# Kernel optimization log

Hardware: AMD Instinct MI355X
Metric: run time of the kernel (lower is better)

The kernel has to match this reference:

```python
import jax, jax.numpy as jnp
import numpy as np

N_ATOMS = 20000
N_PAIRS = 320000
F = 128


def setup_inputs() -> dict:
    key = jax.random.key(0)
    k1, k2, k3, k4, k5 = jax.random.split(key, 5)
    atomic_embedding = jax.random.normal(k1, (N_ATOMS, F), dtype=jnp.float32)
    pairlist = jax.random.randint(k2, (2, N_PAIRS), 0, N_ATOMS)
    f_ij_cutoff = jax.random.uniform(k3, (N_PAIRS, 1), dtype=jnp.float32)
    r_ij = jax.random.normal(k4, (N_PAIRS, 3), dtype=jnp.float32)
    # nn.Linear(F, F) parameters
    W = jax.random.normal(k5, (F, F), dtype=jnp.float32) * (1.0 / np.sqrt(F))
    b = jnp.zeros((F,), dtype=jnp.float32)
    return {"atomic_embedding": atomic_embedding, "pairlist": pairlist,
            "f_ij_cutoff": f_ij_cutoff, "r_ij": r_ij, "W": W, "b": b}


def reference(atomic_embedding, pairlist, f_ij_cutoff, r_ij, W, b):
    n_atoms = atomic_embedding.shape[0]
    idx_i, idx_j = pairlist[0], pairlist[1]
    # gather neighbor embeddings and apply cutoff weight: [P, F]
    a_j = atomic_embedding[idx_j]
    weighted = f_ij_cutoff * a_j
    # scatter-add radial contributions: [N, F]
    radial = jax.ops.segment_sum(weighted, idx_i, num_segments=n_atoms)
    # unit vectors: [P, 3]
    u_ij = r_ij / jnp.linalg.norm(r_ij, axis=1, keepdims=True)
    # outer product per pair: [P, 3, F]
    uwe = u_ij[:, :, None] * weighted[:, None, :]
    # linear layer applied on last dim (y = x @ W^T + b): [P, 3, F]
    transformed = jnp.einsum('pcf,gf->pcg', uwe, W) + b
    # scatter-add vector contributions: [N, 3, F]
    vec = jax.ops.segment_sum(transformed, idx_i, num_segments=n_atoms)
    # norm over the 3 spatial components (eps guards atoms with no pairs): [N, F]
    vector_norms = jnp.sqrt(jnp.sum(vec * vec, axis=1) + 1e-12)
    # combined message: [N, 2F]
    return jnp.concatenate([vector_norms, radial], axis=-1)
```

## Files before the change

kernel.cpp:

```cpp
#include <hip/hip_runtime.h>
#include <hip/hip_bf16.h>

#define FDIM 128
#define CAP 48

typedef short bf16x8 __attribute__((ext_vector_type(8)));
typedef float f32x4  __attribute__((ext_vector_type(4)));

__device__ inline short f2bf_rne(float x) {
    unsigned u = __builtin_bit_cast(unsigned, x);
    u += 0x7FFFu + ((u >> 16) & 1u);
    return (short)(u >> 16);
}
__device__ inline float readlane_f(float v, int l) {
    return __builtin_bit_cast(float, __builtin_amdgcn_readlane(__builtin_bit_cast(int, v), l));
}

__global__ void fill_repack_kernel(const int* __restrict__ pair, const float* __restrict__ fcut,
                                   const float* __restrict__ rij, int* __restrict__ cursor,
                                   int4* __restrict__ rec, const float* __restrict__ W,
                                   short* __restrict__ Wf, int P, int PB) {
    int bx = blockIdx.x;
    if (bx >= PB) {
        int idx = (bx - PB) * 256 + threadIdx.x;
        if (idx < 16384) {
            int j  = idx & 7;
            int l  = (idx >> 3) & 63;
            int tk = idx >> 9;
            int g  = (tk >> 2) * 16 + (l & 15);
            int f  = (tk & 3) * 32 + (l >> 4) * 8 + j;
            Wf[idx] = f2bf_rne(W[g * FDIM + f]);
        }
        return;
    }
    int p = bx * 256 + threadIdx.x;
    if (p >= P) return;
    int i = pair[p], j = pair[P + p];
    float fc = fcut[p];
    float rx = rij[3 * p], ry = rij[3 * p + 1], rz = rij[3 * p + 2];
    float inv = rsqrtf(rx * rx + ry * ry + rz * rz);
    int slot = atomicAdd(&cursor[i], 1);
    if (slot < CAP) {
        int base = (i * CAP + slot) * 2;
        rec[base]     = make_int4(j, 0, 0, 0);
        ((float4*)rec)[base + 1] = make_float4(rx * inv, ry * inv, rz * inv, fc);
    }
}

__global__ __launch_bounds__(256) void fused_kernel(
    const float* __restrict__ A, const int4* __restrict__ rec,
    const int* __restrict__ cursor, const bf16x8* __restrict__ Wfv,
    const float* __restrict__ b, float* __restrict__ out, int N)
{
    __shared__ float sl[4][12][132];
    int wave = __builtin_amdgcn_readfirstlane(threadIdx.x >> 6);
    int lane = threadIdx.x & 63;
    int i0 = blockIdx.x * 16 + wave * 4;
    const float2* A2 = (const float2*)A;
    float cntf[4];

#pragma unroll
    for (int a = 0; a < 4; ++a) {
        int i = i0 + a;
        if (i >= N) { cntf[a] = 0.f; continue; }
        int cnt = __builtin_amdgcn_readfirstlane(min(cursor[i], CAP));
        cntf[a] = (float)cnt;
        int jreg = 0; float ux = 0.f, uy = 0.f, uz = 0.f, fc = 0.f;
        if (lane < cnt) {
            int base = (i * CAP + lane) * 2;
            int4  rj = rec[base];
            float4 ru = ((const float4*)rec)[base + 1];
            jreg = rj.x; ux = ru.x; uy = ru.y; uz = ru.z; fc = ru.w;
        }
        float2 ar = {0.f, 0.f}, ax = {0.f, 0.f}, ay = {0.f, 0.f}, az = {0.f, 0.f};
        for (int k0 = 0; k0 < cnt; k0 += 8) {
            int sj[8]; float sx[8], sy[8], sz[8], sf[8]; float2 aa[8];
#pragma unroll
            for (int q = 0; q < 8; ++q) {
                sj[q] = __builtin_amdgcn_readlane(jreg, k0 + q);
                sx[q] = readlane_f(ux, k0 + q);
                sy[q] = readlane_f(uy, k0 + q);
                sz[q] = readlane_f(uz, k0 + q);
                sf[q] = readlane_f(fc, k0 + q);
            }
#pragma unroll
            for (int q = 0; q < 8; ++q) aa[q] = A2[(size_t)sj[q] * 64 + lane];
#pragma unroll
            for (int q = 0; q < 8; ++q) {
                float wx = sf[q] * aa[q].x, wy = sf[q] * aa[q].y;
                ar.x += wx; ar.y += wy;
                ax.x = fmaf(sx[q], wx, ax.x); ax.y = fmaf(sx[q], wy, ax.y);
                ay.x = fmaf(sy[q], wx, ay.x); ay.y = fmaf(sy[q], wy, ay.y);
                az.x = fmaf(sz[q], wx, az.x); az.y = fmaf(sz[q], wy, az.y);
            }
        }
        ((float2*)&sl[wave][a * 3 + 0][0])[lane] = ax;
        ((float2*)&sl[wave][a * 3 + 1][0])[lane] = ay;
        ((float2*)&sl[wave][a * 3 + 2][0])[lane] = az;
        ((float2*)(out + (size_t)i * 256 + 128))[lane] = ar;
    }

    int m = lane & 15, quad = lane >> 4;
    int mc = min(m, 11);
    bf16x8 a_hi[4], a_lo[4];
    const float* arow = &sl[wave][mc][quad * 8];
#pragma unroll
    for (int kc = 0; kc < 4; ++kc) {
        float4 x0 = *(const float4*)(arow + kc * 32);
        float4 x1 = *(const float4*)(arow + kc * 32 + 4);
        float v[8] = {x0.x, x0.y, x0.z, x0.w, x1.x, x1.y, x1.z, x1.w};
#pragma unroll
        for (int e = 0; e < 8; ++e) {
            float xv = (m < 12) ? v[e] : 0.f;
            unsigned u = __builtin_bit_cast(unsigned, xv);
            float hf = __builtin_bit_cast(float, u & 0xFFFF0000u);
            float r = xv - hf;
            a_hi[kc][e] = (short)(u >> 16);
            a_lo[kc][e] = (short)(__builtin_bit_cast(unsigned, r) >> 16);
        }
    }
    int row0 = quad * 4;
#pragma unroll
    for (int t = 0; t < 8; ++t) {
        f32x4 acc = {0.f, 0.f, 0.f, 0.f};
#pragma unroll
        for (int kc = 0; kc < 4; ++kc) {
            bf16x8 bw = Wfv[(t * 4 + kc) * 64 + lane];
            acc = __builtin_amdgcn_mfma_f32_16x16x32_bf16(a_hi[kc], bw, acc, 0, 0, 0);
            acc = __builtin_amdgcn_mfma_f32_16x16x32_bf16(a_lo[kc], bw, acc, 0, 0, 0);
        }
#pragma unroll
        for (int reg = 0; reg < 4; ++reg) {
            int r = row0 + reg;
            if (r < 12) sl[wave][r][t * 16 + m] = acc[reg];
        }
    }

    float bg0 = b[lane], bg1 = b[lane + 64];
#pragma unroll
    for (int a = 0; a < 4; ++a) {
        int i = i0 + a;
        if (i >= N) continue;
        float t0 = cntf[a] * bg0, t1 = cntf[a] * bg1;
        float v00 = sl[wave][a * 3 + 0][lane] + t0;
        float v10 = sl[wave][a * 3 + 1][lane] + t0;
        float v20 = sl[wave][a * 3 + 2][lane] + t0;
        float v01 = sl[wave][a * 3 + 0][lane + 64] + t1;
        float v11 = sl[wave][a * 3 + 1][lane + 64] + t1;
        float v21 = sl[wave][a * 3 + 2][lane + 64] + t1;
        out[(size_t)i * 256 + lane]      = sqrtf(fmaf(v00, v00, fmaf(v10, v10, fmaf(v20, v20, 1e-12f))));
        out[(size_t)i * 256 + lane + 64] = sqrtf(fmaf(v01, v01, fmaf(v11, v11, fmaf(v21, v21, 1e-12f))));
    }
}

extern "C" void kernel_launch(void* const* d_in, const int* in_sizes, int n_in,
                              void* d_out, int out_size, void* d_ws, size_t ws_size,
                              hipStream_t stream) {
    const float* A    = (const float*)d_in[0];
    const int*   pair = (const int*)d_in[1];
    const float* fcut = (const float*)d_in[2];
    const float* rij  = (const float*)d_in[3];
    const float* W    = (const float*)d_in[4];
    const float* b    = (const float*)d_in[5];
    float* out = (float*)d_out;

    int N = in_sizes[0] / FDIM;
    int P = in_sizes[1] / 2;

    int Npad = ((N + 63) / 64) * 64;
    int*   cursor = (int*)d_ws;
    int4*  rec    = (int4*)(cursor + Npad);
    short* Wf     = (short*)((char*)rec + (size_t)N * CAP * 32);

    int PB = (P + 255) / 256;
    hipMemsetAsync(cursor, 0, (size_t)N * sizeof(int), stream);
    fill_repack_kernel<<<PB + 64, 256, 0, stream>>>(pair, fcut, rij, cursor, rec, W, Wf, P, PB);
    fused_kernel<<<(N + 15) / 16, 256, 0, stream>>>(A, rec, cursor, (const bf16x8*)Wf, b, out, N);
}
```

Before: 127.5 us.

## Shrink bucket records to (j, pair index) and gather geometry in fused kernel

The fill kernel now writes only an 8-byte record (neighbor index, pair index) per slot instead of a 32-byte record holding the unit vector and cutoff. The fused kernel gathers fcut and r_ij by pair index and computes the normalisation itself. All four atoms' records are loaded up front to expose more memory parallelism, and the gather loop is unrolled to 16 neighbors. This cuts scatter-write and reread traffic for the records, at the cost of random gathers of fcut and r_ij in the main kernel and higher register pressure.

```diff
diff --git a/kernel.cpp b/kernel.cpp
--- a/kernel.cpp
+++ b/kernel.cpp
@@ -16,9 +16,8 @@
     return __builtin_bit_cast(float, __builtin_amdgcn_readlane(__builtin_bit_cast(int, v), l));
 }
 
-__global__ void fill_repack_kernel(const int* __restrict__ pair, const float* __restrict__ fcut,
-                                   const float* __restrict__ rij, int* __restrict__ cursor,
-                                   int4* __restrict__ rec, const float* __restrict__ W,
+__global__ void fill_repack_kernel(const int* __restrict__ pair, int* __restrict__ cursor,
+                                   int2* __restrict__ rec, const float* __restrict__ W,
                                    short* __restrict__ Wf, int P, int PB) {
     int bx = blockIdx.x;
     if (bx >= PB) {
@@ -35,21 +34,15 @@
     }
     int p = bx * 256 + threadIdx.x;
     if (p >= P) return;
-    int i = pair[p], j = pair[P + p];
-    float fc = fcut[p];
-    float rx = rij[3 * p], ry = rij[3 * p + 1], rz = rij[3 * p + 2];
-    float inv = rsqrtf(rx * rx + ry * ry + rz * rz);
+    int i = pair[p];
     int slot = atomicAdd(&cursor[i], 1);
-    if (slot < CAP) {
-        int base = (i * CAP + slot) * 2;
-        rec[base]     = make_int4(j, 0, 0, 0);
-        ((float4*)rec)[base + 1] = make_float4(rx * inv, ry * inv, rz * inv, fc);
-    }
+    if (slot < CAP) rec[i * CAP + slot] = make_int2(pair[P + p], p);
 }
 
 __global__ __launch_bounds__(256) void fused_kernel(
-    const float* __restrict__ A, const int4* __restrict__ rec,
-    const int* __restrict__ cursor, const bf16x8* __restrict__ Wfv,
+    const float* __restrict__ A, const int2* __restrict__ rec,
+    const int* __restrict__ cursor, const float* __restrict__ fcut,
+    const float* __restrict__ rij, const bf16x8* __restrict__ Wfv,
     const float* __restrict__ b, float* __restrict__ out, int N)
 {
     __shared__ float sl[4][12][132];
@@ -57,41 +50,56 @@
     int lane = threadIdx.x & 63;
     int i0 = blockIdx.x * 16 + wave * 4;
     const float2* A2 = (const float2*)A;
-    float cntf[4];
 
+    int cnts[4], jreg[4], preg[4];
+    float uxr[4], uyr[4], uzr[4], fcr[4];
 #pragma unroll
     for (int a = 0; a < 4; ++a) {
         int i = i0 + a;
-        if (i >= N) { cntf[a] = 0.f; continue; }
-        int cnt = __builtin_amdgcn_readfirstlane(min(cursor[i], CAP));
-        cntf[a] = (float)cnt;
-        int jreg = 0; float ux = 0.f, uy = 0.f, uz = 0.f, fc = 0.f;
-        if (lane < cnt) {
-            int base = (i * CAP + lane) * 2;
-            int4  rj = rec[base];
-            float4 ru = ((const float4*)rec)[base + 1];
-            jreg = rj.x; ux = ru.x; uy = ru.y; uz = ru.z; fc = ru.w;
+        int cnt = (i < N) ? min(cursor[i], CAP) : 0;
+        cnt = __builtin_amdgcn_readfirstlane(cnt);
+        cnts[a] = cnt;
+        int2 r = make_int2(0, 0);
+        if (lane < cnt) r = rec[i * CAP + lane];
+        jreg[a] = r.x; preg[a] = r.y;
+    }
+#pragma unroll
+    for (int a = 0; a < 4; ++a) {
+        float fc = 0.f, rx = 0.f, ry = 0.f, rz = 1.f;
+        if (lane < cnts[a]) {
+            int p = preg[a];
+            fc = fcut[p];
+            rx = rij[3 * p]; ry = rij[3 * p + 1]; rz = rij[3 * p + 2];
         }
+        float inv = rsqrtf(rx * rx + ry * ry + rz * rz);
+        uxr[a] = rx * inv; uyr[a] = ry * inv; uzr[a] = rz * inv; fcr[a] = fc;
+    }
+
+    float cntf[4];
+#pragma unroll
+    for (int a = 0; a < 4; ++a) {
+        int i = i0 + a;
+        cntf[a] = (float)cnts[a];
+        if (i >= N) continue;
+        int cnt = cnts[a];
         float2 ar = {0.f, 0.f}, ax = {0.f, 0.f}, ay = {0.f, 0.f}, az = {0.f, 0.f};
-        for (int k0 = 0; k0 < cnt; k0 += 8) {
-            int sj[8]; float sx[8], sy[8], sz[8], sf[8]; float2 aa[8];
+        for (int k0 = 0; k0 < cnt; k0 += 16) {
+            int sj[16]; float2 aa[16];
 #pragma unroll
-            for (int q = 0; q < 8; ++q) {
-                sj[q] = __builtin_amdgcn_readlane(jreg, k0 + q);
-                sx[q] = readlane_f(ux, k0 + q);
-                sy[q] = readlane_f(uy, k0 + q);
-                sz[q] = readlane_f(uz, k0 + q);
-                sf[q] = readlane_f(fc, k0 + q);
-            }
+            for (int q = 0; q < 16; ++q) sj[q] = __builtin_amdgcn_readlane(jreg[a], k0 + q);
 #pragma unroll
-            for (int q = 0; q < 8; ++q) aa[q] = A2[(size_t)sj[q] * 64 + lane];
+            for (int q = 0; q < 16; ++q) aa[q] = A2[(size_t)sj[q] * 64 + lane];
 #pragma unroll
-            for (int q = 0; q < 8; ++q) {
-                float wx = sf[q] * aa[q].x, wy = sf[q] * aa[q].y;
+            for (int q = 0; q < 16; ++q) {
+                float sx = readlane_f(uxr[a], k0 + q);
+                float sy = readlane_f(uyr[a], k0 + q);
+                float sz = readlane_f(uzr[a], k0 + q);
+                float sf = readlane_f(fcr[a], k0 + q);
+                float wx = sf * aa[q].x, wy = sf * aa[q].y;
                 ar.x += wx; ar.y += wy;
-                ax.x = fmaf(sx[q], wx, ax.x); ax.y = fmaf(sx[q], wy, ax.y);
-                ay.x = fmaf(sy[q], wx, ay.x); ay.y = fmaf(sy[q], wy, ay.y);
-                az.x = fmaf(sz[q], wx, az.x); az.y = fmaf(sz[q], wy, az.y);
+                ax.x = fmaf(sx, wx, ax.x); ax.y = fmaf(sx, wy, ax.y);
+                ay.x = fmaf(sy, wx, ay.x); ay.y = fmaf(sy, wy, ay.y);
+                az.x = fmaf(sz, wx, az.x); az.y = fmaf(sz, wy, az.y);
             }
         }
         ((float2*)&sl[wave][a * 3 + 0][0])[lane] = ax;
@@ -169,11 +177,12 @@
 
     int Npad = ((N + 63) / 64) * 64;
     int*   cursor = (int*)d_ws;
-    int4*  rec    = (int4*)(cursor + Npad);
-    short* Wf     = (short*)((char*)rec + (size_t)N * CAP * 32);
+    int2*  rec    = (int2*)(cursor + Npad);
+    short* Wf     = (short*)((char*)rec + (size_t)N * CAP * 8);
 
     int PB = (P + 255) / 256;
     hipMemsetAsync(cursor, 0, (size_t)N * sizeof(int), stream);
-    fill_repack_kernel<<<PB + 64, 256, 0, stream>>>(pair, fcut, rij, cursor, rec, W, Wf, P, PB);
-    fused_kernel<<<(N + 15) / 16, 256, 0, stream>>>(A, rec, cursor, (const bf16x8*)Wf, b, out, N);
+    fill_repack_kernel<<<PB + 64, 256, 0, stream>>>(pair, cursor, rec, W, Wf, P, PB);
+    fused_kernel<<<(N + 15) / 16, 256, 0, stream>>>(A, rec, cursor, fcut, rij,
+                                                    (const bf16x8*)Wf, b, out, N);
 }
```

New measurement: 132.5 us. 1.04x slower.

## Gather bf16 copy of atom embeddings and split pair records into compact arrays

Applied to the files above, without the earlier changes.

Adds a pre-pass that converts the atomic embedding table to bf16, so the per-pair neighbor gather in the fused kernel reads half as many bytes per row. The 32-byte padded pair record is also split into a separate int index array and a float4 array, which shrinks record storage and traffic. The cost is an extra conversion pass over the embeddings, plus reduced precision in both the radial sum and the vector sum (embeddings now rounded to bf16), which may push the result past tolerance.

```diff
diff --git a/kernel.cpp b/kernel.cpp
--- a/kernel.cpp
+++ b/kernel.cpp
@@ -7,10 +7,10 @@
 typedef short bf16x8 __attribute__((ext_vector_type(8)));
 typedef float f32x4  __attribute__((ext_vector_type(4)));
 
-__device__ inline short f2bf_rne(float x) {
+__device__ inline unsigned f2bf_rne_u(float x) {
     unsigned u = __builtin_bit_cast(unsigned, x);
     u += 0x7FFFu + ((u >> 16) & 1u);
-    return (short)(u >> 16);
+    return u >> 16;
 }
 __device__ inline float readlane_f(float v, int l) {
     return __builtin_bit_cast(float, __builtin_amdgcn_readlane(__builtin_bit_cast(int, v), l));
@@ -18,9 +18,22 @@
 
 __global__ void fill_repack_kernel(const int* __restrict__ pair, const float* __restrict__ fcut,
                                    const float* __restrict__ rij, int* __restrict__ cursor,
-                                   int4* __restrict__ rec, const float* __restrict__ W,
-                                   short* __restrict__ Wf, int P, int PB) {
+                                   int* __restrict__ j_s, float4* __restrict__ ufc,
+                                   const float* __restrict__ W, short* __restrict__ Wf,
+                                   const float4* __restrict__ A4, uint2* __restrict__ Abf2,
+                                   int P, int N, int PB) {
     int bx = blockIdx.x;
+    if (bx >= PB + 64) {
+        int idx = (bx - PB - 64) * 256 + threadIdx.x;
+        if (idx < N * 32) {
+            float4 v = A4[idx];
+            uint2 o;
+            o.x = f2bf_rne_u(v.x) | (f2bf_rne_u(v.y) << 16);
+            o.y = f2bf_rne_u(v.z) | (f2bf_rne_u(v.w) << 16);
+            Abf2[idx] = o;
+        }
+        return;
+    }
     if (bx >= PB) {
         int idx = (bx - PB) * 256 + threadIdx.x;
         if (idx < 16384) {
@@ -29,7 +42,7 @@
             int tk = idx >> 9;
             int g  = (tk >> 2) * 16 + (l & 15);
             int f  = (tk & 3) * 32 + (l >> 4) * 8 + j;
-            Wf[idx] = f2bf_rne(W[g * FDIM + f]);
+            Wf[idx] = (short)f2bf_rne_u(W[g * FDIM + f]);
         }
         return;
     }
@@ -41,22 +54,21 @@
     float inv = rsqrtf(rx * rx + ry * ry + rz * rz);
     int slot = atomicAdd(&cursor[i], 1);
     if (slot < CAP) {
-        int base = (i * CAP + slot) * 2;
-        rec[base]     = make_int4(j, 0, 0, 0);
-        ((float4*)rec)[base + 1] = make_float4(rx * inv, ry * inv, rz * inv, fc);
+        j_s[i * CAP + slot] = j;
+        ufc[i * CAP + slot] = make_float4(rx * inv, ry * inv, rz * inv, fc);
     }
 }
 
 __global__ __launch_bounds__(256) void fused_kernel(
-    const float* __restrict__ A, const int4* __restrict__ rec,
-    const int* __restrict__ cursor, const bf16x8* __restrict__ Wfv,
-    const float* __restrict__ b, float* __restrict__ out, int N)
+    const unsigned* __restrict__ Abf, const int* __restrict__ j_s,
+    const float4* __restrict__ ufc, const int* __restrict__ cursor,
+    const bf16x8* __restrict__ Wfv, const float* __restrict__ b,
+    float* __restrict__ out, int N)
 {
     __shared__ float sl[4][12][132];
     int wave = __builtin_amdgcn_readfirstlane(threadIdx.x >> 6);
     int lane = threadIdx.x & 63;
     int i0 = blockIdx.x * 16 + wave * 4;
-    const float2* A2 = (const float2*)A;
     float cntf[4];
 
 #pragma unroll
@@ -67,14 +79,13 @@
         cntf[a] = (float)cnt;
         int jreg = 0; float ux = 0.f, uy = 0.f, uz = 0.f, fc = 0.f;
         if (lane < cnt) {
-            int base = (i * CAP + lane) * 2;
-            int4  rj = rec[base];
-            float4 ru = ((const float4*)rec)[base + 1];
-            jreg = rj.x; ux = ru.x; uy = ru.y; uz = ru.z; fc = ru.w;
+            jreg = j_s[i * CAP + lane];
+            float4 ru = ufc[i * CAP + lane];
+            ux = ru.x; uy = ru.y; uz = ru.z; fc = ru.w;
         }
         float2 ar = {0.f, 0.f}, ax = {0.f, 0.f}, ay = {0.f, 0.f}, az = {0.f, 0.f};
         for (int k0 = 0; k0 < cnt; k0 += 8) {
-            int sj[8]; float sx[8], sy[8], sz[8], sf[8]; float2 aa[8];
+            int sj[8]; float sx[8], sy[8], sz[8], sf[8]; unsigned aa[8];
 #pragma unroll
             for (int q = 0; q < 8; ++q) {
                 sj[q] = __builtin_amdgcn_readlane(jreg, k0 + q);
@@ -84,10 +95,12 @@
                 sf[q] = readlane_f(fc, k0 + q);
             }
 #pragma unroll
-            for (int q = 0; q < 8; ++q) aa[q] = A2[(size_t)sj[q] * 64 + lane];
+            for (int q = 0; q < 8; ++q) aa[q] = Abf[(size_t)sj[q] * 64 + lane];
 #pragma unroll
             for (int q = 0; q < 8; ++q) {
-                float wx = sf[q] * aa[q].x, wy = sf[q] * aa[q].y;
+                float a0 = __builtin_bit_cast(float, aa[q] << 16);
+                float a1 = __builtin_bit_cast(float, aa[q] & 0xFFFF0000u);
+                float wx = sf[q] * a0, wy = sf[q] * a1;
                 ar.x += wx; ar.y += wy;
                 ax.x = fmaf(sx[q], wx, ax.x); ax.y = fmaf(sx[q], wy, ax.y);
                 ay.x = fmaf(sy[q], wx, ay.x); ay.y = fmaf(sy[q], wy, ay.y);
@@ -168,12 +181,18 @@
     int P = in_sizes[1] / 2;
 
     int Npad = ((N + 63) / 64) * 64;
-    int*   cursor = (int*)d_ws;
-    int4*  rec    = (int4*)(cursor + Npad);
-    short* Wf     = (short*)((char*)rec + (size_t)N * CAP * 32);
+    int*      cursor = (int*)d_ws;
+    int*      j_s    = cursor + Npad;
+    float4*   ufc    = (float4*)(j_s + (size_t)N * CAP);
+    short*    Wf     = (short*)(ufc + (size_t)N * CAP);
+    unsigned* Abf    = (unsigned*)(Wf + 16384);
 
     int PB = (P + 255) / 256;
+    int ACB = (N * 32 + 255) / 256;
     hipMemsetAsync(cursor, 0, (size_t)N * sizeof(int), stream);
-    fill_repack_kernel<<<PB + 64, 256, 0, stream>>>(pair, fcut, rij, cursor, rec, W, Wf, P, PB);
-    fused_kernel<<<(N + 15) / 16, 256, 0, stream>>>(A, rec, cursor, (const bf16x8*)Wf, b, out, N);
+    fill_repack_kernel<<<PB + 64 + ACB, 256, 0, stream>>>(
+        pair, fcut, rij, cursor, j_s, ufc, W, Wf,
+        (const float4*)A, (uint2*)Abf, P, N, PB);
+    fused_kernel<<<(N + 15) / 16, 256, 0, stream>>>(Abf, j_s, ufc, cursor,
+                                                    (const bf16x8*)Wf, b, out, N);
 }
```

Measured after the change: 129.2 us. About the same (+1.4%).
